# Kernel tuning notes

Hardware: AMD Instinct MI355X
Metric: run time of the kernel (lower is better)

## Reference

```python
import jax, jax.numpy as jnp
import numpy as np

N_NODES = 20000
N_EDGES = 100000
WALK_LEN = 4
FEAT_DIM = 256
HID = 64
NUM_HEAD = 8
H_RNN = NUM_HEAD * HID  # 512
OUT_DIM = 16


def setup_inputs() -> dict:
    key = jax.random.key(0)
    ks = jax.random.split(key, 12)
    s = 0.05  # small init scale for numerical stability
    return {
        "x": jax.random.normal(ks[0], (N_NODES, FEAT_DIM), jnp.float32),
        "W_mlp": jax.random.normal(ks[1], (HID, FEAT_DIM), jnp.float32) * s,
        "b_mlp": jnp.zeros((HID,), jnp.float32),
        "W_ih": jax.random.normal(ks[2], (3 * H_RNN, HID), jnp.float32) * s,
        "W_hh": jax.random.normal(ks[3], (3 * H_RNN, H_RNN), jnp.float32) * s,
        "b_ih": jnp.zeros((3 * H_RNN,), jnp.float32),
        "b_hh": jnp.zeros((3 * H_RNN,), jnp.float32),
        "attn": jax.random.normal(ks[4], (1, NUM_HEAD, HID), jnp.float32) * s,
        "W_emb": jax.random.normal(ks[5], (HID, H_RNN), jnp.float32) * s,
        "b_emb": jnp.zeros((HID,), jnp.float32),
        "W_last": jax.random.normal(ks[6], (OUT_DIM, HID), jnp.float32) * s,
        "b_last": jnp.zeros((OUT_DIM,), jnp.float32),
        "edge_metapath_indices": jax.random.randint(ks[7], (N_EDGES, WALK_LEN), 0, N_NODES),
        "num_nodes": N_NODES,
    }


def reference(x, W_mlp, b_mlp, W_ih, W_hh, b_ih, b_hh, attn, W_emb, b_emb,
              W_last, b_last, edge_metapath_indices, num_nodes):
    # self channel: embedding = mlp(data.x)
    emb = x @ W_mlp.T + b_mlp                       # [N, hid]

    # rnn channel: gather per-metapath node embeddings
    edata = emb[edge_metapath_indices]              # [E, L, hid]
    E = edata.shape[0]
    h_rnn = W_hh.shape[1]

    # torch nn.GRU cell (gate order r, z, n), scan over path length
    def gru_step(h, x_t):
        xg = x_t @ W_ih.T + b_ih                    # [E, 3H]
        hg = h @ W_hh.T + b_hh                      # [E, 3H]
        xr, xz, xn = jnp.split(xg, 3, axis=-1)
        hr, hz, hn = jnp.split(hg, 3, axis=-1)
        r = jax.nn.sigmoid(xr + hr)
        z = jax.nn.sigmoid(xz + hz)
        n = jnp.tanh(xn + r * hn)
        return (1.0 - z) * n + z * h, None

    h0 = jnp.zeros((E, h_rnn), edata.dtype)
    hT, _ = jax.lax.scan(gru_step, h0, jnp.swapaxes(edata, 0, 1))  # [E, 8*hid]

    num_head, hid = attn.shape[1], attn.shape[2]
    eft = hT.reshape(E, num_head, hid)              # per-edge features

    # attention logits + leaky_relu(0.01)
    a = jnp.sum(eft * attn, axis=-1)                # [E, num_head]
    a = jnp.where(a > 0, a, 0.01 * a)

    # edge softmax grouped by destination node (indices[:, -1])
    dst = edge_metapath_indices[:, -1]
    m = jax.ops.segment_max(a, dst, num_segments=num_nodes)        # [N, H]
    ea = jnp.exp(a - m[dst])
    ssum = jax.ops.segment_sum(ea, dst, num_segments=num_nodes)    # [N, H]
    alpha = ea / ssum[dst]                          # [E, H]

    # message passing: scatter-sum of attention-weighted edge features
    ft = jax.ops.segment_sum(eft * alpha[:, :, None], dst,
                             num_segments=num_nodes)               # [N, H, hid]
    ret = ft.reshape(num_nodes, num_head * hid)
    rnn_emb = ret @ W_emb.T + b_emb                 # [N, hid]

    out = rnn_emb @ W_last.T + b_last               # [N, out_dim]
    return out
```

## Files before the change

kernel.cpp:

```cpp
#include <hip/hip_runtime.h>
#include <hip/hip_bf16.h>
#include <cstdint>

#define N_NODES 20000
#define N_EDGES 100000
#define WALK 4
#define FDIM 256
#define HID 64
#define NHEAD 8
#define HR 512
#define OUTD 16

typedef __attribute__((ext_vector_type(8))) short bf16x8;
typedef __attribute__((ext_vector_type(8))) unsigned short u16x8;
typedef __attribute__((ext_vector_type(4))) float f32x4;

__device__ __forceinline__ float b2f(unsigned short u){
  union{float f; unsigned u;} x; x.u = ((unsigned)u)<<16; return x.f;
}
__device__ __forceinline__ unsigned short f2b(float f){
  union{float f; unsigned u;} x; x.f = f;
  unsigned r = x.u + 0x7FFFu + ((x.u>>16)&1u);
  return (unsigned short)(r>>16);
}
__device__ __forceinline__ float sigmoidf_(float v){ return 1.0f/(1.0f+__expf(-v)); }
__device__ __forceinline__ float tanh_c(float v){
  v = fminf(fmaxf(v, -15.f), 15.f);
  const float t2 = __expf(2.0f*v);
  return (t2 - 1.0f) / (t2 + 1.0f);
}

__device__ __forceinline__ void gload16(const void* g, void* l){
  __builtin_amdgcn_global_load_lds(
      (const __attribute__((address_space(1))) void*)(g),
      (__attribute__((address_space(3))) void*)(l),
      16, 0, 0);
}

__device__ __forceinline__ f32x4 mfma16(bf16x8 a, bf16x8 b, f32x4 c){
  return __builtin_amdgcn_mfma_f32_16x16x32_bf16(a, b, c, 0, 0, 0);
}

__launch_bounds__(256)
__global__ void emb_kernel(const float* __restrict__ x,
                           const float* __restrict__ Wm,
                           const float* __restrict__ bm,
                           unsigned short* __restrict__ emb_bf)
{
  __shared__ float xs[4][FDIM];
  const int tid = threadIdx.x;
  const int node0 = blockIdx.x * 4;
  {
    const int row = tid >> 6;
    const int k4  = (tid & 63) * 4;
    *reinterpret_cast<float4*>(&xs[row][k4]) =
      *reinterpret_cast<const float4*>(&x[(size_t)(node0+row)*FDIM + k4]);
  }
  __syncthreads();
  const int nn = tid >> 6, c = tid & 63;
  float acc = bm[c];
  const float* wr = &Wm[c*FDIM];
  #pragma unroll 8
  for (int k=0;k<FDIM;k+=4){
    const float4 w = *reinterpret_cast<const float4*>(&wr[k]);
    acc += xs[nn][k]*w.x + xs[nn][k+1]*w.y + xs[nn][k+2]*w.z + xs[nn][k+3]*w.w;
  }
  emb_bf[(size_t)(node0+nn)*HID + c] = f2b(acc);
}

__launch_bounds__(256)
__global__ void prep_kernel(const float* __restrict__ Whh,
                            const float* __restrict__ Wih,
                            const float* __restrict__ Wemb,
                            unsigned short* __restrict__ WhhP,
                            unsigned short* __restrict__ WihP,
                            unsigned short* __restrict__ WembP)
{
  const int t = blockIdx.x*256 + threadIdx.x;
  if (t < 8*192*512){
    const int k = t & 511;
    const int r = (t >> 9) % 192;
    const int db = t / 98304;
    const int f = r >> 4, fr = r & 15;
    const int g = f % 3, dgrp = f / 3;
    const int G = g*HR + db*64 + dgrp*16 + fr;
    const int kg = k >> 6, kw = k & 63;
    const int c = kw >> 3, o = kw & 7;
    const int ksrc = (kg<<6) + (((c ^ (r&7)) << 3) | o);
    WhhP[t] = f2b(Whh[(size_t)G*HR + ksrc]);
  }
  if (t < 8*192*64){
    const int k = t & 63;
    const int r = (t >> 6) % 192;
    const int db = t / 12288;
    const int f = r >> 4, fr = r & 15;
    const int g = f % 3, dgrp = f / 3;
    const int G = g*HR + db*64 + dgrp*16 + fr;
    const int c = k >> 3, o = k & 7;
    const int ksrc = (((c ^ (r&7)) << 3) | o);
    WihP[t] = f2b(Wih[(size_t)G*HID + ksrc]);
  }
  if (t < 64*512){
    const int k = t & 511;
    const int o = t >> 9;
    const int kg = k >> 6, kw = k & 63;
    const int c = kw >> 3, off = kw & 7;
    const int ksrc = (kg<<6) + (((c ^ (o&7)) << 3) | off);
    WembP[t] = f2b(Wemb[(size_t)o*HR + ksrc]);
  }
}

__launch_bounds__(512)
__global__ void xg_kernel(const unsigned short* __restrict__ emb_bf,
                          const unsigned short* __restrict__ WihP,
                          const float* __restrict__ b_ih,
                          const float* __restrict__ b_hh,
                          unsigned short* __restrict__ xnP,
                          unsigned short* __restrict__ h1n)
{
  __shared__ __align__(16) char smem[32768 + 24576];
  char* Ab = smem;
  char* Bb = smem + 32768;
  const int tid = threadIdx.x, lane = tid & 63, w = tid >> 6;
  const int wr = w >> 1, wn = w & 1;
  const int n0 = blockIdx.x * 256;
  const int db = blockIdx.y;

  #pragma unroll
  for (int j=0;j<4;++j){
    const int flat = j*512 + tid;
    const int row = flat >> 3, c = flat & 7;
    int n = n0 + row; if (n > N_NODES-1) n = N_NODES-1;
    gload16(emb_bf + ((size_t)n*HID + ((c ^ (row&7))<<3)), Ab + ((j*512 + w*64)<<4));
  }
  #pragma unroll
  for (int j=0;j<3;++j){
    const int flat = j*512 + tid;
    const int row = flat >> 3, c = flat & 7;
    gload16(WihP + ((size_t)(db*192 + row)*HID + c*8), Bb + ((j*512 + w*64)<<4));
  }
  asm volatile("s_waitcnt vmcnt(0)" ::: "memory");
  __builtin_amdgcn_s_barrier();

  f32x4 acc[4][6];
  #pragma unroll
  for (int m=0;m<4;++m)
    #pragma unroll
    for (int f=0;f<6;++f) acc[m][f] = (f32x4)(0.f);

  auto readFrag = [&](const char* base, int row, int kk)->bf16x8{
    const int chunk = (kk<<2) + (lane>>4);
    return *reinterpret_cast<const bf16x8*>(base + (row<<7) + ((chunk ^ (row&7))<<4));
  };
  #pragma unroll
  for (int kk=0; kk<2; ++kk){
    bf16x8 a_[4];
    #pragma unroll
    for (int mf=0; mf<4; ++mf) a_[mf] = readFrag(Ab, wr*64 + mf*16 + (lane&15), kk);
    #pragma unroll
    for (int nf=0; nf<6; ++nf){
      const bf16x8 b_ = readFrag(Bb, wn*96 + nf*16 + (lane&15), kk);
      #pragma unroll
      for (int mf=0; mf<4; ++mf) acc[mf][nf] = mfma16(a_[mf], b_, acc[mf][nf]);
    }
  }

  const int fr_ = lane & 15;
  #pragma unroll
  for (int mf=0; mf<4; ++mf){
    #pragma unroll
    for (int reg=0; reg<4; ++reg){
      const int row = wr*64 + mf*16 + ((lane>>4)<<2) + reg;
      const int n = n0 + row;
      if (n < N_NODES){
        #pragma unroll
        for (int t=0; t<2; ++t){
          const int d6 = (2*wn+t)*16 + fr_;
          const int dG = db*64 + d6;
          const float xr = acc[mf][t*3+0][reg] + b_ih[dG];
          const float xz = acc[mf][t*3+1][reg] + b_ih[HR+dG];
          const float xn = acc[mf][t*3+2][reg] + b_ih[2*HR+dG];
          xnP[((size_t)db*N_NODES + n)*64 + d6] = f2b(xn);
          const float r = sigmoidf_(xr + b_hh[dG]);
          const float z = sigmoidf_(xz + b_hh[HR+dG]);
          const float nn = tanh_c(xn + r*b_hh[2*HR+dG]);
          h1n[(size_t)n*HR + dG] = f2b((1.0f - z)*nn);
        }
      }
    }
  }
}

template<int STEP, bool SCORE>
__launch_bounds__(512, 2)
__global__ void gru_mfma(const unsigned short* __restrict__ emb_bf,
                         const int* __restrict__ idx,
                         const unsigned short* __restrict__ h_in,
                         unsigned short* __restrict__ h_out,
                         const unsigned short* __restrict__ WhhP,
                         const unsigned short* __restrict__ WihP,
                         const unsigned short* __restrict__ xnP,
                         const float* __restrict__ b_ih,
                         const float* __restrict__ b_hh,
                         const float* __restrict__ attn,
                         float* __restrict__ a_buf)
{
  constexpr bool GATHER = (STEP == 1);
  __shared__ __align__(16) char smem[3*32768 + 2*24576];

  const int tid = threadIdx.x;
  const int lane = tid & 63;
  const int w = tid >> 6;
  const int wr = w >> 1, wn = w & 1;

  const int bid = blockIdx.x;
  const int sid = (bid & 7)*391 + (bid >> 3);
  const int et = sid >> 3;
  const int db = sid & 7;
  const int e0 = et * 256;

  f32x4 acc[4][6];
  #pragma unroll
  for (int m=0;m<4;++m)
    #pragma unroll
    for (int f=0;f<6;++f) acc[m][f] = (f32x4)(0.f);

  auto Abase = [&](int s)->char*{ return smem + s*32768; };
  auto Bbase = [&](int s)->char*{ return smem + 98304 + s*24576; };

  auto stage_A = [&](int slot, int kt){
    #pragma unroll
    for (int j=0;j<4;++j){
      const int flat = j*512 + tid;
      const int row = flat >> 3, c = flat & 7;
      int e = e0 + row; if (e > N_EDGES-1) e = N_EDGES-1;
      const unsigned short* src;
      if (kt == 8){
        const int node = idx[e*WALK + STEP];
        src = emb_bf + ((size_t)node*HID + ((c ^ (row&7)) << 3));
      } else if (GATHER){
        const int node = idx[e*WALK];
        src = h_in + ((size_t)node*HR + kt*64 + ((c ^ (row&7)) << 3));
      } else {
        src = h_in + ((size_t)e*HR + kt*64 + c*8);
      }
      gload16(src, Abase(slot) + ((j*512 + w*64) << 4));
    }
  };
  auto stage_B = [&](int slot, int kt){
    #pragma unroll
    for (int j=0;j<3;++j){
      const int flat = j*512 + tid;
      const int row = flat >> 3, c = flat & 7;
      const unsigned short* src = (kt < 8)
        ? WhhP + ((size_t)(db*192 + row)*HR + kt*64 + c*8)
        : WihP + ((size_t)(db*192 + row)*HID + c*8);
      gload16(src, Bbase(slot) + ((j*512 + w*64) << 4));
    }
  };

  auto readFrag = [&](const char* base, int row, int kk)->bf16x8{
    const int chunk = (kk<<2) + (lane>>4);
    return *reinterpret_cast<const bf16x8*>(base + (row<<7) + ((chunk ^ (row&7))<<4));
  };

#define COMPUTE(ab, bb, kk, XS)                                               \
  {                                                                           \
    bf16x8 a_[4];                                                             \
    _Pragma("unroll")                                                         \
    for (int mf=0; mf<4; ++mf)                                                \
      a_[mf] = readFrag(ab, wr*64 + mf*16 + (lane&15), kk);                   \
    __builtin_amdgcn_s_setprio(1);                                            \
    _Pragma("unroll")                                                         \
    for (int nf=0; nf<6; ++nf){                                               \
      if (XS && (nf % 3) == 2) continue;                                      \
      const bf16x8 b_ = readFrag(bb, wn*96 + nf*16 + (lane&15), kk);          \
      _Pragma("unroll")                                                       \
      for (int mf=0; mf<4; ++mf)                                              \
        acc[mf][nf] = mfma16(a_[mf], b_, acc[mf][nf]);                        \
    }                                                                         \
    __builtin_amdgcn_s_setprio(0);                                            \
  }

  stage_A(0, 0); stage_B(0, 0); stage_A(1, 1);
  asm volatile("s_waitcnt vmcnt(4)" ::: "memory");
  __builtin_amdgcn_s_barrier();
  __builtin_amdgcn_sched_barrier(0);

  #pragma unroll
  for (int kt=0; kt<9; ++kt){
    char* ab = Abase(kt%3);
    char* bb = Bbase(kt&1);
    if (kt+1 < 9) stage_B((kt+1)&1, kt+1);
    if (kt==8){ COMPUTE(ab, bb, 0, true);  } else { COMPUTE(ab, bb, 0, false); }
    if (kt+2 < 9) stage_A((kt+2)%3, kt+2);
    if (kt==8){ COMPUTE(ab, bb, 1, true);  } else { COMPUTE(ab, bb, 1, false); }
    if (kt < 8){
      if (kt < 7) asm volatile("s_waitcnt vmcnt(4)" ::: "memory");
      else        asm volatile("s_waitcnt vmcnt(0)" ::: "memory");
      __builtin_amdgcn_s_barrier();
      __builtin_amdgcn_sched_barrier(0);
    }
  }
#undef COMPUTE

  const int fr_ = lane & 15;
  float bhr[2], bhz[2], bhn[2], at[2];
  #pragma unroll
  for (int t=0; t<2; ++t){
    const int d6 = (2*wn+t)*16 + fr_;
    const int dG = db*64 + d6;
    bhr[t] = b_ih[dG]      + b_hh[dG];
    bhz[t] = b_ih[HR+dG]   + b_hh[HR+dG];
    bhn[t] = b_hh[2*HR+dG];
    at[t]  = SCORE ? attn[db*HID + d6] : 0.f;
  }

  #pragma unroll
  for (int mf=0; mf<4; ++mf){
    #pragma unroll
    for (int reg=0; reg<4; ++reg){
      const int row = wr*64 + mf*16 + ((lane>>4)<<2) + reg;
      const int e = e0 + row;
      float sp = 0.f;
      if (e < N_EDGES){
        const int4 iv = *reinterpret_cast<const int4*>(&idx[e*WALK]);
        const int nodeS = (STEP==1) ? iv.y : ((STEP==2) ? iv.z : iv.w);
        #pragma unroll
        for (int t=0; t<2; ++t){
          const int d6 = (2*wn+t)*16 + fr_;
          const int dG = db*64 + d6;
          const float xn = b2f(xnP[((size_t)db*N_NODES + nodeS)*64 + d6]);
          float hold;
          if (GATHER) hold = b2f(h_in[(size_t)iv.x*HR + dG]);
          else        hold = b2f(h_in[(size_t)e*HR + db*64 + (((d6>>3) ^ (e&7))<<3) + (d6&7)]);
          const float r  = sigmoidf_(acc[mf][t*3+0][reg] + bhr[t]);
          const float z  = sigmoidf_(acc[mf][t*3+1][reg] + bhz[t]);
          const float hn = acc[mf][t*3+2][reg] + bhn[t];
          const float nn = tanh_c(xn + r*hn);
          const float hv = (1.0f - z)*nn + z*hold;
          h_out[(size_t)e*HR + db*64 + (((d6>>3) ^ (e&7))<<3) + (d6&7)] = f2b(hv);
          if (SCORE) sp += hv * at[t];
        }
      }
      if (SCORE){
        sp += __shfl_xor(sp, 1);
        sp += __shfl_xor(sp, 2);
        sp += __shfl_xor(sp, 4);
        sp += __shfl_xor(sp, 8);
        if (fr_ == 0 && e < N_EDGES)
          atomicAdd(&a_buf[e*NHEAD + db], sp);
      }
    }
  }
}

__launch_bounds__(256)
__global__ void score2_kernel(const int* __restrict__ idx,
                              float* __restrict__ a_buf,
                              unsigned int* __restrict__ mmax)
{
  const int flat = blockIdx.x*256 + threadIdx.x;
  const int e = flat >> 3, h = flat & 7;
  const float s = a_buf[flat];
  const float a = s > 0.f ? s : 0.01f*s;
  a_buf[flat] = a;
  const int dst = idx[e*WALK + 3];
  union{float f; unsigned u;} x; x.f = a;
  const unsigned key = (x.u & 0x80000000u) ? ~x.u : (x.u | 0x80000000u);
  atomicMax(&mmax[dst*NHEAD + h], key);
}

__launch_bounds__(256)
__global__ void ea_kernel(const int* __restrict__ idx,
                          float* __restrict__ a_buf,
                          const unsigned int* __restrict__ mmax,
                          float* __restrict__ ssum)
{
  const int flat = blockIdx.x*256 + threadIdx.x;
  const int e = flat >> 3, h = flat & 7;
  const int dst = idx[e*WALK + 3];
  const unsigned key = mmax[dst*NHEAD + h];
  union{float f; unsigned u;} x;
  x.u = (key & 0x80000000u) ? (key & 0x7FFFFFFFu) : ~key;
  const float ea = __expf(a_buf[flat] - x.f);
  a_buf[flat] = ea;
  atomicAdd(&ssum[dst*NHEAD + h], ea);
}

__launch_bounds__(256)
__global__ void alpha_kernel(const int* __restrict__ idx,
                             float* __restrict__ a_buf,
                             const float* __restrict__ ssum)
{
  const int flat = blockIdx.x*256 + threadIdx.x;
  const int e = flat >> 3, h = flat & 7;
  const int dst = idx[e*WALK + 3];
  a_buf[flat] = a_buf[flat] / ssum[dst*NHEAD + h];
}

__launch_bounds__(256)
__global__ void z_kernel(const unsigned short* __restrict__ hT,
                         const int* __restrict__ idx,
                         const float* __restrict__ alpha,
                         const unsigned short* __restrict__ WembP,
                         float* __restrict__ zacc)
{
  __shared__ __align__(16) char zs[40960];
  char* Az = zs;
  char* Bz = zs + 32768;
  const int tid = threadIdx.x;
  const int lane = tid & 63;
  const int w = tid >> 6;
  const int e0 = blockIdx.x * 256;

  f32x4 acc[4][4];
  #pragma unroll
  for (int m=0;m<4;++m)
    #pragma unroll
    for (int f=0;f<4;++f) acc[m][f] = (f32x4)(0.f);

  auto readFrag = [&](const char* base, int row, int kk)->bf16x8{
    const int chunk = (kk<<2) + (lane>>4);
    return *reinterpret_cast<const bf16x8*>(base + (row<<7) + ((chunk ^ (row&7))<<4));
  };

  #pragma unroll 1
  for (int kt=0; kt<8; ++kt){
    __syncthreads();
    #pragma unroll
    for (int j=0;j<8;++j){
      const int flat = j*256 + tid;
      const int row = flat >> 3, c = flat & 7;
      int e = e0 + row; if (e > N_EDGES-1) e = N_EDGES-1;
      const u16x8 hv = *reinterpret_cast<const u16x8*>(hT + (size_t)e*HR + kt*64 + c*8);
      const float al = alpha[e*NHEAD + kt];
      union { bf16x8 v; unsigned short s[8]; } o;
      #pragma unroll
      for (int i=0;i<8;++i) o.s[i] = f2b(b2f(hv[i]) * al);
      *reinterpret_cast<bf16x8*>(Az + flat*16) = o.v;
    }
    #pragma unroll
    for (int j=0;j<2;++j){
      const int flat = j*256 + tid;
      const int row = flat >> 3, c = flat & 7;
      gload16(WembP + ((size_t)row*HR + kt*64 + c*8), Bz + ((j*256 + w*64)<<4));
    }
    __syncthreads();
    #pragma unroll
    for (int kk=0; kk<2; ++kk){
      bf16x8 a_[4];
      #pragma unroll
      for (int mf=0; mf<4; ++mf)
        a_[mf] = readFrag(Az, w*64 + mf*16 + (lane&15), kk);
      #pragma unroll
      for (int nf=0; nf<4; ++nf){
        const bf16x8 b_ = readFrag(Bz, nf*16 + (lane&15), kk);
        #pragma unroll
        for (int mf=0; mf<4; ++mf)
          acc[mf][nf] = mfma16(a_[mf], b_, acc[mf][nf]);
      }
    }
  }

  #pragma unroll
  for (int mf=0; mf<4; ++mf){
    #pragma unroll
    for (int reg=0; reg<4; ++reg){
      const int row = w*64 + mf*16 + ((lane>>4)<<2) + reg;
      const int e = e0 + row;
      if (e < N_EDGES){
        const int dst = idx[e*WALK + 3];
        #pragma unroll
        for (int nf=0; nf<4; ++nf){
          const int o = nf*16 + (lane&15);
          atomicAdd(&zacc[(size_t)dst*64 + o], acc[mf][nf][reg]);
        }
      }
    }
  }
}

__launch_bounds__(256)
__global__ void out2_kernel(const float* __restrict__ zacc,
                            const float* __restrict__ b_emb,
                            const float* __restrict__ W_last,
                            const float* __restrict__ b_last,
                            float* __restrict__ out)
{
  const int flat = blockIdx.x*256 + threadIdx.x;
  if (flat >= N_NODES*OUTD) return;
  const int n = flat >> 4, o = flat & 15;
  float s = b_last[o];
  const float* zr = &zacc[(size_t)n*64];
  const float* wl = &W_last[o*64];
  #pragma unroll
  for (int k=0;k<64;++k) s += (zr[k] + b_emb[k]) * wl[k];
  out[(size_t)n*OUTD + o] = s;
}

extern "C" void kernel_launch(void* const* d_in, const int* in_sizes, int n_in,
                              void* d_out, int out_size, void* d_ws, size_t ws_size,
                              hipStream_t stream)
{
  (void)in_sizes; (void)n_in; (void)out_size; (void)ws_size;
  const float* x      = (const float*)d_in[0];
  const float* W_mlp  = (const float*)d_in[1];
  const float* b_mlp  = (const float*)d_in[2];
  const float* W_ih   = (const float*)d_in[3];
  const float* W_hh   = (const float*)d_in[4];
  const float* b_ih   = (const float*)d_in[5];
  const float* b_hh   = (const float*)d_in[6];
  const float* attn   = (const float*)d_in[7];
  const float* W_emb  = (const float*)d_in[8];
  const float* b_emb  = (const float*)d_in[9];
  const float* W_last = (const float*)d_in[10];
  const float* b_last = (const float*)d_in[11];
  const int*   idx    = (const int*)d_in[12];
  float* out = (float*)d_out;

  char* ws = (char*)d_ws;
  unsigned short* WhhP   = (unsigned short*)(ws + 0);
  unsigned short* WihP   = (unsigned short*)(ws + 1572864);
  unsigned short* WembP  = (unsigned short*)(ws + 1769472);
  unsigned short* emb_bf = (unsigned short*)(ws + 1835008);
  unsigned short* xnP    = (unsigned short*)(ws + 4395008);
  float*          a_buf  = (float*)(ws + 24875008);
  unsigned int*   mmax   = (unsigned int*)(ws + 28075008);
  float*          ssum   = (float*)(ws + 28715008);
  float*          zacc   = (float*)(ws + 29355008);
  unsigned short* h_a    = (unsigned short*)(ws + 34475008);
  unsigned short* h_b    = (unsigned short*)(ws + 136875008);
  unsigned short* h1n    = h_b;

  hipMemsetAsync(a_buf, 0, 9600000, stream);

  prep_kernel<<<3072, 256, 0, stream>>>(W_hh, W_ih, W_emb, WhhP, WihP, WembP);
  emb_kernel<<<N_NODES/4, 256, 0, stream>>>(x, W_mlp, b_mlp, emb_bf);

  dim3 xgrid(79, 8);
  xg_kernel<<<xgrid, 512, 0, stream>>>(emb_bf, WihP, b_ih, b_hh, xnP, h1n);

  const int NWG = 391*8;
  gru_mfma<1,false><<<NWG, 512, 0, stream>>>(emb_bf, idx, h1n, h_a, WhhP, WihP, xnP, b_ih, b_hh, attn, a_buf);
  gru_mfma<2,false><<<NWG, 512, 0, stream>>>(emb_bf, idx, h_a, h_b, WhhP, WihP, xnP, b_ih, b_hh, attn, a_buf);
  gru_mfma<3,true ><<<NWG, 512, 0, stream>>>(emb_bf, idx, h_b, h_a, WhhP, WihP, xnP, b_ih, b_hh, attn, a_buf);

  score2_kernel<<<N_EDGES*NHEAD/256, 256, 0, stream>>>(idx, a_buf, mmax);
  ea_kernel<<<N_EDGES*NHEAD/256, 256, 0, stream>>>(idx, a_buf, mmax, ssum);
  alpha_kernel<<<N_EDGES*NHEAD/256, 256, 0, stream>>>(idx, a_buf, ssum);
  z_kernel<<<391, 256, 0, stream>>>(h_a, idx, a_buf, WembP, zacc);
  out2_kernel<<<(N_NODES*OUTD+255)/256, 256, 0, stream>>>(zacc, b_emb, W_last, b_last, out);
}
```

Baseline: 1.299 ms.

## Halve GRU edge tile, double-buffer LDS, stage epilogue through LDS for vector stores

The GRU step kernel moves from a 256-edge tile with triple-buffered A to a 128-edge tile with double-buffered A/B, cutting LDS to 80KB and raising launch bounds to 4 blocks per CU. Gather indices are hoisted out of the k-loop into registers. The epilogue now transposes accumulators through LDS so each thread handles one edge and 8 contiguous features, which gives 16-byte vectorized loads and stores and one attention atomic per edge-head instead of a shuffle reduction. In exchange, B-weight reuse per block is halved, so weight traffic doubles, and prefetch depth drops to a single stage with a full vmcnt(0) wait every iteration.

```diff
diff --git a/kernel.cpp b/kernel.cpp
--- a/kernel.cpp
+++ b/kernel.cpp
@@ -192,7 +192,7 @@
 }
 
 template<int STEP, bool SCORE>
-__launch_bounds__(512, 2)
+__launch_bounds__(512, 4)
 __global__ void gru_mfma(const unsigned short* __restrict__ emb_bf,
                          const int* __restrict__ idx,
                          const unsigned short* __restrict__ h_in,
@@ -206,7 +206,7 @@
                          float* __restrict__ a_buf)
 {
   constexpr bool GATHER = (STEP == 1);
-  __shared__ __align__(16) char smem[3*32768 + 2*24576];
+  __shared__ __align__(16) char smem[81920];
 
   const int tid = threadIdx.x;
   const int lane = tid & 63;
@@ -214,35 +214,42 @@
   const int wr = w >> 1, wn = w & 1;
 
   const int bid = blockIdx.x;
-  const int sid = (bid & 7)*391 + (bid >> 3);
+  const int sid = (bid & 7)*782 + (bid >> 3);
   const int et = sid >> 3;
   const int db = sid & 7;
-  const int e0 = et * 256;
-
-  f32x4 acc[4][6];
-  #pragma unroll
-  for (int m=0;m<4;++m)
+  const int e0 = et * 128;
+
+  int eS[2], nH[2], nX[2];
+  #pragma unroll
+  for (int j=0;j<2;++j){
+    int e = e0 + ((j*512 + tid) >> 3);
+    if (e > N_EDGES-1) e = N_EDGES-1;
+    eS[j] = e;
+    nX[j] = idx[e*WALK + STEP];
+    nH[j] = GATHER ? idx[e*WALK] : 0;
+  }
+
+  f32x4 acc[2][6];
+  #pragma unroll
+  for (int m=0;m<2;++m)
     #pragma unroll
     for (int f=0;f<6;++f) acc[m][f] = (f32x4)(0.f);
 
-  auto Abase = [&](int s)->char*{ return smem + s*32768; };
-  auto Bbase = [&](int s)->char*{ return smem + 98304 + s*24576; };
+  auto Abase = [&](int s)->char*{ return smem + s*16384; };
+  auto Bbase = [&](int s)->char*{ return smem + 32768 + s*24576; };
 
   auto stage_A = [&](int slot, int kt){
     #pragma unroll
-    for (int j=0;j<4;++j){
+    for (int j=0;j<2;++j){
       const int flat = j*512 + tid;
       const int row = flat >> 3, c = flat & 7;
-      int e = e0 + row; if (e > N_EDGES-1) e = N_EDGES-1;
       const unsigned short* src;
       if (kt == 8){
-        const int node = idx[e*WALK + STEP];
-        src = emb_bf + ((size_t)node*HID + ((c ^ (row&7)) << 3));
+        src = emb_bf + ((size_t)nX[j]*HID + ((c ^ (row&7)) << 3));
       } else if (GATHER){
-        const int node = idx[e*WALK];
-        src = h_in + ((size_t)node*HR + kt*64 + ((c ^ (row&7)) << 3));
+        src = h_in + ((size_t)nH[j]*HR + kt*64 + ((c ^ (row&7)) << 3));
       } else {
-        src = h_in + ((size_t)e*HR + kt*64 + c*8);
+        src = h_in + ((size_t)eS[j]*HR + kt*64 + c*8);
       }
       gload16(src, Abase(slot) + ((j*512 + w*64) << 4));
     }
@@ -266,92 +273,128 @@
 
 #define COMPUTE(ab, bb, kk, XS)                                               \
   {                                                                           \
-    bf16x8 a_[4];                                                             \
+    bf16x8 a_[2];                                                             \
     _Pragma("unroll")                                                         \
-    for (int mf=0; mf<4; ++mf)                                                \
-      a_[mf] = readFrag(ab, wr*64 + mf*16 + (lane&15), kk);                   \
+    for (int mf=0; mf<2; ++mf)                                                \
+      a_[mf] = readFrag(ab, wr*32 + mf*16 + (lane&15), kk);                   \
     __builtin_amdgcn_s_setprio(1);                                            \
     _Pragma("unroll")                                                         \
     for (int nf=0; nf<6; ++nf){                                               \
       if (XS && (nf % 3) == 2) continue;                                      \
       const bf16x8 b_ = readFrag(bb, wn*96 + nf*16 + (lane&15), kk);          \
       _Pragma("unroll")                                                       \
-      for (int mf=0; mf<4; ++mf)                                              \
+      for (int mf=0; mf<2; ++mf)                                              \
         acc[mf][nf] = mfma16(a_[mf], b_, acc[mf][nf]);                        \
     }                                                                         \
     __builtin_amdgcn_s_setprio(0);                                            \
   }
 
-  stage_A(0, 0); stage_B(0, 0); stage_A(1, 1);
-  asm volatile("s_waitcnt vmcnt(4)" ::: "memory");
+  stage_A(0, 0); stage_B(0, 0);
+  asm volatile("s_waitcnt vmcnt(0)" ::: "memory");
   __builtin_amdgcn_s_barrier();
   __builtin_amdgcn_sched_barrier(0);
 
   #pragma unroll
   for (int kt=0; kt<9; ++kt){
-    char* ab = Abase(kt%3);
-    char* bb = Bbase(kt&1);
-    if (kt+1 < 9) stage_B((kt+1)&1, kt+1);
+    const int buf = kt & 1;
+    char* ab = Abase(buf);
+    char* bb = Bbase(buf);
+    if (kt < 8){ stage_A(buf^1, kt+1); stage_B(buf^1, kt+1); }
     if (kt==8){ COMPUTE(ab, bb, 0, true);  } else { COMPUTE(ab, bb, 0, false); }
-    if (kt+2 < 9) stage_A((kt+2)%3, kt+2);
     if (kt==8){ COMPUTE(ab, bb, 1, true);  } else { COMPUTE(ab, bb, 1, false); }
     if (kt < 8){
-      if (kt < 7) asm volatile("s_waitcnt vmcnt(4)" ::: "memory");
-      else        asm volatile("s_waitcnt vmcnt(0)" ::: "memory");
+      asm volatile("s_waitcnt vmcnt(0)" ::: "memory");
       __builtin_amdgcn_s_barrier();
       __builtin_amdgcn_sched_barrier(0);
     }
   }
 #undef COMPUTE
 
-  const int fr_ = lane & 15;
-  float bhr[2], bhz[2], bhn[2], at[2];
-  #pragma unroll
-  for (int t=0; t<2; ++t){
-    const int d6 = (2*wn+t)*16 + fr_;
-    const int dG = db*64 + d6;
-    bhr[t] = b_ih[dG]      + b_hh[dG];
-    bhz[t] = b_ih[HR+dG]   + b_hh[HR+dG];
-    bhn[t] = b_hh[2*HR+dG];
-    at[t]  = SCORE ? attn[db*HID + d6] : 0.f;
-  }
-
-  #pragma unroll
-  for (int mf=0; mf<4; ++mf){
-    #pragma unroll
-    for (int reg=0; reg<4; ++reg){
-      const int row = wr*64 + mf*16 + ((lane>>4)<<2) + reg;
-      const int e = e0 + row;
-      float sp = 0.f;
-      if (e < N_EDGES){
-        const int4 iv = *reinterpret_cast<const int4*>(&idx[e*WALK]);
-        const int nodeS = (STEP==1) ? iv.y : ((STEP==2) ? iv.z : iv.w);
+  float* EX = (float*)smem;
+  const int eL = tid & 127;
+  const int c4 = tid >> 7;
+  const int tt = c4 >> 1;
+  const int fr0 = (c4 & 1) * 8;
+  const int eg = e0 + eL;
+  const int ec = (eg > N_EDGES-1) ? (N_EDGES-1) : eg;
+  float spart = 0.f;
+
+  __syncthreads();
+
+  #pragma unroll
+  for (int p=0; p<2; ++p){
+    if (p) __syncthreads();
+    if (wn == p){
+      #pragma unroll
+      for (int mf=0; mf<2; ++mf){
+        const int rc = wr*8 + mf*4 + (lane>>4);
         #pragma unroll
-        for (int t=0; t<2; ++t){
-          const int d6 = (2*wn+t)*16 + fr_;
-          const int dG = db*64 + d6;
-          const float xn = b2f(xnP[((size_t)db*N_NODES + nodeS)*64 + d6]);
-          float hold;
-          if (GATHER) hold = b2f(h_in[(size_t)iv.x*HR + dG]);
-          else        hold = b2f(h_in[(size_t)e*HR + db*64 + (((d6>>3) ^ (e&7))<<3) + (d6&7)]);
-          const float r  = sigmoidf_(acc[mf][t*3+0][reg] + bhr[t]);
-          const float z  = sigmoidf_(acc[mf][t*3+1][reg] + bhz[t]);
-          const float hn = acc[mf][t*3+2][reg] + bhn[t];
-          const float nn = tanh_c(xn + r*hn);
-          const float hv = (1.0f - z)*nn + z*hold;
-          h_out[(size_t)e*HR + db*64 + (((d6>>3) ^ (e&7))<<3) + (d6&7)] = f2b(hv);
-          if (SCORE) sp += hv * at[t];
+        for (int nf=0; nf<6; ++nf){
+          const int cl = nf*16 + (lane&15);
+          *reinterpret_cast<f32x4*>((char*)EX + cl*512 + ((rc ^ (cl&7))<<4)) = acc[mf][nf];
         }
       }
-      if (SCORE){
-        sp += __shfl_xor(sp, 1);
-        sp += __shfl_xor(sp, 2);
-        sp += __shfl_xor(sp, 4);
-        sp += __shfl_xor(sp, 8);
-        if (fr_ == 0 && e < N_EDGES)
-          atomicAdd(&a_buf[e*NHEAD + db], sp);
-      }
-    }
+    }
+    __syncthreads();
+
+    const int d60 = p*32 + c4*8;
+    const int dG0 = db*64 + d60;
+
+    float gr[8], gz[8], gn[8];
+    #pragma unroll
+    for (int i=0;i<8;++i){
+      const int clr = (tt*3+0)*16 + fr0 + i;
+      const int clz = (tt*3+1)*16 + fr0 + i;
+      const int cln = (tt*3+2)*16 + fr0 + i;
+      const int psw = ((eL>>2) ^ i) << 4;
+      const int wo  = (eL&3) * 4;
+      gr[i] = *reinterpret_cast<const float*>((char*)EX + clr*512 + psw + wo);
+      gz[i] = *reinterpret_cast<const float*>((char*)EX + clz*512 + psw + wo);
+      gn[i] = *reinterpret_cast<const float*>((char*)EX + cln*512 + psw + wo);
+    }
+
+    float bir[8], biz[8], bhn[8];
+    #pragma unroll
+    for (int i=0;i<8;++i){
+      bir[i] = b_ih[dG0+i]      + b_hh[dG0+i];
+      biz[i] = b_ih[HR+dG0+i]   + b_hh[HR+dG0+i];
+      bhn[i] = b_hh[2*HR+dG0+i];
+    }
+
+    const int nodeS = idx[ec*WALK + STEP];
+    const u16x8 xnv = *reinterpret_cast<const u16x8*>(
+        xnP + ((size_t)db*N_NODES + nodeS)*64 + d60);
+    u16x8 hov;
+    if (GATHER){
+      const int nodeH = idx[ec*WALK];
+      hov = *reinterpret_cast<const u16x8*>(h_in + (size_t)nodeH*HR + dG0);
+    } else {
+      const int cidx = d60 >> 3;
+      hov = *reinterpret_cast<const u16x8*>(
+          h_in + (size_t)ec*HR + db*64 + ((cidx ^ (ec&7))<<3));
+    }
+
+    union { u16x8 v; unsigned short s[8]; } outp;
+    #pragma unroll
+    for (int i=0;i<8;++i){
+      const float r  = sigmoidf_(gr[i] + bir[i]);
+      const float z  = sigmoidf_(gz[i] + biz[i]);
+      const float hn = gn[i] + bhn[i];
+      const float xn = b2f(xnv[i]);
+      const float nn = tanh_c(xn + r*hn);
+      const float hv = (1.0f - z)*nn + z*b2f(hov[i]);
+      outp.s[i] = f2b(hv);
+      if (SCORE) spart += hv * attn[dG0 + i];
+    }
+    if (eg < N_EDGES){
+      const int cidx = d60 >> 3;
+      *reinterpret_cast<u16x8*>(
+          h_out + (size_t)eg*HR + db*64 + ((cidx ^ (eg&7))<<3)) = outp.v;
+    }
+  }
+
+  if (SCORE && eg < N_EDGES){
+    atomicAdd(&a_buf[eg*NHEAD + db], spart);
   }
 }
 
@@ -541,7 +584,7 @@
   dim3 xgrid(79, 8);
   xg_kernel<<<xgrid, 512, 0, stream>>>(emb_bf, WihP, b_ih, b_hh, xnP, h1n);
 
-  const int NWG = 391*8;
+  const int NWG = 782*8;
   gru_mfma<1,false><<<NWG, 512, 0, stream>>>(emb_bf, idx, h1n, h_a, WhhP, WihP, xnP, b_ih, b_hh, attn, a_buf);
   gru_mfma<2,false><<<NWG, 512, 0, stream>>>(emb_bf, idx, h_a, h_b, WhhP, WihP, xnP, b_ih, b_hh, attn, a_buf);
   gru_mfma<3,true ><<<NWG, 512, 0, stream>>>(emb_bf, idx, h_b, h_a, WhhP, WihP, xnP, b_ih, b_hh, attn, a_buf);
```

Measured after the change: 1.340 ms. +3.2%, slower.

## Fuse three GRU step kernels into one with the hidden state kept in LDS

Applied to the files above, without the earlier changes.

Replaces the three per-step GRU MFMA launches with a single kernel. Each block owns 64 edges, keeps their 512-wide hidden state in shared memory across all three steps, and writes only the final state to global memory. The input-gate projections for all three gates are now precomputed per node in xg_kernel and gathered in the epilogue, instead of folding W_ih into the GEMM K-loop. This removes the global write/read round trips of the hidden state between steps. In exchange, every block streams the full W_hh once per step, which greatly increases weight traffic. The smaller per-wave MFMA tiles, the barrier on every K-slice and the large LDS footprint (limiting occupancy) may also cut throughput.

```diff
diff --git a/kernel.cpp b/kernel.cpp
--- a/kernel.cpp
+++ b/kernel.cpp
@@ -115,7 +115,7 @@
                           const unsigned short* __restrict__ WihP,
                           const float* __restrict__ b_ih,
                           const float* __restrict__ b_hh,
-                          unsigned short* __restrict__ xnP,
+                          unsigned short* __restrict__ xgP,
                           unsigned short* __restrict__ h1n)
 {
   __shared__ __align__(16) char smem[32768 + 24576];
@@ -180,7 +180,9 @@
           const float xr = acc[mf][t*3+0][reg] + b_ih[dG];
           const float xz = acc[mf][t*3+1][reg] + b_ih[HR+dG];
           const float xn = acc[mf][t*3+2][reg] + b_ih[2*HR+dG];
-          xnP[((size_t)db*N_NODES + n)*64 + d6] = f2b(xn);
+          xgP[(size_t)n*1536 + dG]        = f2b(xr);
+          xgP[(size_t)n*1536 + 512 + dG]  = f2b(xz);
+          xgP[(size_t)n*1536 + 1024 + dG] = f2b(xn);
           const float r = sigmoidf_(xr + b_hh[dG]);
           const float z = sigmoidf_(xz + b_hh[HR+dG]);
           const float nn = tanh_c(xn + r*b_hh[2*HR+dG]);
@@ -191,166 +193,169 @@
   }
 }
 
-template<int STEP, bool SCORE>
 __launch_bounds__(512, 2)
-__global__ void gru_mfma(const unsigned short* __restrict__ emb_bf,
-                         const int* __restrict__ idx,
-                         const unsigned short* __restrict__ h_in,
-                         unsigned short* __restrict__ h_out,
-                         const unsigned short* __restrict__ WhhP,
-                         const unsigned short* __restrict__ WihP,
-                         const unsigned short* __restrict__ xnP,
-                         const float* __restrict__ b_ih,
-                         const float* __restrict__ b_hh,
-                         const float* __restrict__ attn,
-                         float* __restrict__ a_buf)
-{
-  constexpr bool GATHER = (STEP == 1);
-  __shared__ __align__(16) char smem[3*32768 + 2*24576];
-
-  const int tid = threadIdx.x;
-  const int lane = tid & 63;
-  const int w = tid >> 6;
-  const int wr = w >> 1, wn = w & 1;
-
-  const int bid = blockIdx.x;
-  const int sid = (bid & 7)*391 + (bid >> 3);
-  const int et = sid >> 3;
-  const int db = sid & 7;
-  const int e0 = et * 256;
-
-  f32x4 acc[4][6];
-  #pragma unroll
-  for (int m=0;m<4;++m)
-    #pragma unroll
-    for (int f=0;f<6;++f) acc[m][f] = (f32x4)(0.f);
-
-  auto Abase = [&](int s)->char*{ return smem + s*32768; };
-  auto Bbase = [&](int s)->char*{ return smem + 98304 + s*24576; };
-
-  auto stage_A = [&](int slot, int kt){
-    #pragma unroll
-    for (int j=0;j<4;++j){
-      const int flat = j*512 + tid;
-      const int row = flat >> 3, c = flat & 7;
-      int e = e0 + row; if (e > N_EDGES-1) e = N_EDGES-1;
-      const unsigned short* src;
-      if (kt == 8){
-        const int node = idx[e*WALK + STEP];
-        src = emb_bf + ((size_t)node*HID + ((c ^ (row&7)) << 3));
-      } else if (GATHER){
-        const int node = idx[e*WALK];
-        src = h_in + ((size_t)node*HR + kt*64 + ((c ^ (row&7)) << 3));
-      } else {
-        src = h_in + ((size_t)e*HR + kt*64 + c*8);
-      }
-      gload16(src, Abase(slot) + ((j*512 + w*64) << 4));
-    }
+__global__ void gru_fused(const int* __restrict__ idx,
+                          const unsigned short* __restrict__ h1n,
+                          const unsigned short* __restrict__ WhhP,
+                          const unsigned short* __restrict__ xgP,
+                          const float* __restrict__ b_hh,
+                          const float* __restrict__ attn,
+                          unsigned short* __restrict__ hT,
+                          float* __restrict__ a_buf)
+{
+  __shared__ __align__(16) char smem[147456];
+  char* const hL = smem;
+  float* const biasT = (float*)(smem + 139264);
+  float* const attnT = (float*)(smem + 145408);
+
+  const int tid = threadIdx.x, lane = tid & 63, w = tid >> 6;
+  const int lrow = lane & 15, lkg = lane >> 4;
+  const int rg = w >> 2, dgrp = w & 3;
+  const int e0 = blockIdx.x * 64;
+
+  auto Bbuf = [&](int s)->char*{ return smem + 65536 + s*24576; };
+
+  biasT[tid]      = b_hh[tid];
+  biasT[512+tid]  = b_hh[HR+tid];
+  biasT[1024+tid] = b_hh[2*HR+tid];
+  attnT[tid]      = attn[tid];
+
+  #pragma unroll
+  for (int j=0;j<8;++j){
+    const int flat = j*512 + tid;
+    const int row = flat >> 6, c64 = flat & 63;
+    int e = e0 + row; if (e > N_EDGES-1) e = N_EDGES-1;
+    const int n0 = idx[e*WALK];
+    const u16x8 v = *reinterpret_cast<const u16x8*>(h1n + (size_t)n0*HR + c64*8);
+    *reinterpret_cast<u16x8*>(hL + row*1024 + (c64>>3)*128 + (((c64&7) ^ (row&7))<<4)) = v;
+  }
+  __syncthreads();
+
+  auto readA = [&](int row, int kt, int kk)->bf16x8{
+    return *reinterpret_cast<const bf16x8*>(
+        hL + row*1024 + kt*128 + (((lkg + kk*4) ^ (row&7))<<4));
   };
-  auto stage_B = [&](int slot, int kt){
+  auto readB = [&](const char* bb, int r, int kk)->bf16x8{
+    return *reinterpret_cast<const bf16x8*>(
+        bb + r*128 + (((lkg + kk*4) ^ (r&7))<<4));
+  };
+  auto stageB = [&](int slot, int db, int kt){
     #pragma unroll
     for (int j=0;j<3;++j){
       const int flat = j*512 + tid;
-      const int row = flat >> 3, c = flat & 7;
-      const unsigned short* src = (kt < 8)
-        ? WhhP + ((size_t)(db*192 + row)*HR + kt*64 + c*8)
-        : WihP + ((size_t)(db*192 + row)*HID + c*8);
-      gload16(src, Bbase(slot) + ((j*512 + w*64) << 4));
+      const int r = flat >> 3, c = flat & 7;
+      gload16(WhhP + ((size_t)(db*192 + r)*HR + kt*64 + c*8),
+              Bbuf(slot) + ((j*512 + w*64) << 4));
     }
   };
 
-  auto readFrag = [&](const char* base, int row, int kk)->bf16x8{
-    const int chunk = (kk<<2) + (lane>>4);
-    return *reinterpret_cast<const bf16x8*>(base + (row<<7) + ((chunk ^ (row&7))<<4));
-  };
-
-#define COMPUTE(ab, bb, kk, XS)                                               \
-  {                                                                           \
-    bf16x8 a_[4];                                                             \
-    _Pragma("unroll")                                                         \
-    for (int mf=0; mf<4; ++mf)                                                \
-      a_[mf] = readFrag(ab, wr*64 + mf*16 + (lane&15), kk);                   \
-    __builtin_amdgcn_s_setprio(1);                                            \
-    _Pragma("unroll")                                                         \
-    for (int nf=0; nf<6; ++nf){                                               \
-      if (XS && (nf % 3) == 2) continue;                                      \
-      const bf16x8 b_ = readFrag(bb, wn*96 + nf*16 + (lane&15), kk);          \
-      _Pragma("unroll")                                                       \
-      for (int mf=0; mf<4; ++mf)                                              \
-        acc[mf][nf] = mfma16(a_[mf], b_, acc[mf][nf]);                        \
-    }                                                                         \
-    __builtin_amdgcn_s_setprio(0);                                            \
-  }
-
-  stage_A(0, 0); stage_B(0, 0); stage_A(1, 1);
-  asm volatile("s_waitcnt vmcnt(4)" ::: "memory");
-  __builtin_amdgcn_s_barrier();
-  __builtin_amdgcn_sched_barrier(0);
-
-  #pragma unroll
-  for (int kt=0; kt<9; ++kt){
-    char* ab = Abase(kt%3);
-    char* bb = Bbase(kt&1);
-    if (kt+1 < 9) stage_B((kt+1)&1, kt+1);
-    if (kt==8){ COMPUTE(ab, bb, 0, true);  } else { COMPUTE(ab, bb, 0, false); }
-    if (kt+2 < 9) stage_A((kt+2)%3, kt+2);
-    if (kt==8){ COMPUTE(ab, bb, 1, true);  } else { COMPUTE(ab, bb, 1, false); }
-    if (kt < 8){
-      if (kt < 7) asm volatile("s_waitcnt vmcnt(4)" ::: "memory");
-      else        asm volatile("s_waitcnt vmcnt(0)" ::: "memory");
-      __builtin_amdgcn_s_barrier();
-      __builtin_amdgcn_sched_barrier(0);
-    }
-  }
-#undef COMPUTE
-
-  const int fr_ = lane & 15;
-  float bhr[2], bhz[2], bhn[2], at[2];
-  #pragma unroll
-  for (int t=0; t<2; ++t){
-    const int d6 = (2*wn+t)*16 + fr_;
-    const int dG = db*64 + d6;
-    bhr[t] = b_ih[dG]      + b_hh[dG];
-    bhz[t] = b_ih[HR+dG]   + b_hh[HR+dG];
-    bhn[t] = b_hh[2*HR+dG];
-    at[t]  = SCORE ? attn[db*HID + d6] : 0.f;
-  }
-
-  #pragma unroll
-  for (int mf=0; mf<4; ++mf){
-    #pragma unroll
-    for (int reg=0; reg<4; ++reg){
-      const int row = wr*64 + mf*16 + ((lane>>4)<<2) + reg;
-      const int e = e0 + row;
-      float sp = 0.f;
-      if (e < N_EDGES){
-        const int4 iv = *reinterpret_cast<const int4*>(&idx[e*WALK]);
-        const int nodeS = (STEP==1) ? iv.y : ((STEP==2) ? iv.z : iv.w);
-        #pragma unroll
-        for (int t=0; t<2; ++t){
-          const int d6 = (2*wn+t)*16 + fr_;
-          const int dG = db*64 + d6;
-          const float xn = b2f(xnP[((size_t)db*N_NODES + nodeS)*64 + d6]);
-          float hold;
-          if (GATHER) hold = b2f(h_in[(size_t)iv.x*HR + dG]);
-          else        hold = b2f(h_in[(size_t)e*HR + db*64 + (((d6>>3) ^ (e&7))<<3) + (d6&7)]);
-          const float r  = sigmoidf_(acc[mf][t*3+0][reg] + bhr[t]);
-          const float z  = sigmoidf_(acc[mf][t*3+1][reg] + bhz[t]);
-          const float hn = acc[mf][t*3+2][reg] + bhn[t];
-          const float nn = tanh_c(xn + r*hn);
-          const float hv = (1.0f - z)*nn + z*hold;
-          h_out[(size_t)e*HR + db*64 + (((d6>>3) ^ (e&7))<<3) + (d6&7)] = f2b(hv);
-          if (SCORE) sp += hv * at[t];
+  float hsv[8][8];
+
+  #pragma unroll 1
+  for (int t=1; t<WALK; ++t){
+    int nodes[2][4];
+    #pragma unroll
+    for (int mf=0;mf<2;++mf)
+      #pragma unroll
+      for (int reg=0;reg<4;++reg){
+        int e = e0 + rg*32 + mf*16 + lkg*4 + reg;
+        if (e > N_EDGES-1) e = N_EDGES-1;
+        nodes[mf][reg] = idx[e*WALK + t];
+      }
+
+    #pragma unroll
+    for (int db=0; db<8; ++db){
+      f32x4 acc[2][3];
+      #pragma unroll
+      for (int m=0;m<2;++m)
+        #pragma unroll
+        for (int g=0;g<3;++g) acc[m][g] = (f32x4)(0.f);
+
+      stageB(0, db, 0); stageB(1, db, 1);
+
+      #pragma unroll 1
+      for (int kt=0; kt<8; ++kt){
+        if (kt == 7) asm volatile("s_waitcnt vmcnt(0)" ::: "memory");
+        else         asm volatile("s_waitcnt vmcnt(3)" ::: "memory");
+        __builtin_amdgcn_s_barrier();
+        __builtin_amdgcn_sched_barrier(0);
+        if (kt + 2 < 8) stageB((kt+2)%3, db, kt+2);
+        char* bb = Bbuf(kt%3);
+        #pragma unroll
+        for (int kk=0; kk<2; ++kk){
+          const bf16x8 a0 = readA(rg*32 + lrow,      kt, kk);
+          const bf16x8 a1 = readA(rg*32 + 16 + lrow, kt, kk);
+          __builtin_amdgcn_s_setprio(1);
+          #pragma unroll
+          for (int g=0; g<3; ++g){
+            const bf16x8 b_ = readB(bb, (dgrp*3+g)*16 + lrow, kk);
+            acc[0][g] = mfma16(a0, b_, acc[0][g]);
+            acc[1][g] = mfma16(a1, b_, acc[1][g]);
+          }
+          __builtin_amdgcn_s_setprio(0);
         }
       }
-      if (SCORE){
-        sp += __shfl_xor(sp, 1);
-        sp += __shfl_xor(sp, 2);
-        sp += __shfl_xor(sp, 4);
-        sp += __shfl_xor(sp, 8);
-        if (fr_ == 0 && e < N_EDGES)
-          atomicAdd(&a_buf[e*NHEAD + db], sp);
+      __builtin_amdgcn_s_barrier();
+
+      const int col = db*64 + dgrp*16 + lrow;
+      const float br = biasT[col], bz = biasT[512+col], bn = biasT[1024+col];
+      const float av = attnT[col];
+      #pragma unroll
+      for (int mf=0;mf<2;++mf){
+        #pragma unroll
+        for (int reg=0;reg<4;++reg){
+          const int row = rg*32 + mf*16 + lkg*4 + reg;
+          const int node = nodes[mf][reg];
+          const size_t xb = (size_t)node*1536 + col;
+          const float xr = b2f(xgP[xb]);
+          const float xz = b2f(xgP[xb + 512]);
+          const float xn = b2f(xgP[xb + 1024]);
+          const float hold = b2f(*reinterpret_cast<const unsigned short*>(
+              hL + row*1024 + db*128 + ((((col>>3)&7) ^ (row&7))<<4) + (col&7)*2));
+          const float r  = sigmoidf_(xr + acc[mf][0][reg] + br);
+          const float z  = sigmoidf_(xz + acc[mf][1][reg] + bz);
+          const float nn = tanh_c(xn + r*(acc[mf][2][reg] + bn));
+          const float hv = (1.0f - z)*nn + z*hold;
+          hsv[db][mf*4+reg] = hv;
+          if (t == WALK-1){
+            float s = hv * av;
+            s += __shfl_xor(s, 1);
+            s += __shfl_xor(s, 2);
+            s += __shfl_xor(s, 4);
+            s += __shfl_xor(s, 8);
+            const int e = e0 + row;
+            if (lrow == mf*4+reg && e < N_EDGES)
+              atomicAdd(&a_buf[e*NHEAD + db], s);
+          }
+        }
       }
+    }
+
+    __syncthreads();
+    #pragma unroll
+    for (int db=0; db<8; ++db){
+      const int col = db*64 + dgrp*16 + lrow;
+      #pragma unroll
+      for (int mf=0;mf<2;++mf)
+        #pragma unroll
+        for (int reg=0;reg<4;++reg){
+          const int row = rg*32 + mf*16 + lkg*4 + reg;
+          *reinterpret_cast<unsigned short*>(
+              hL + row*1024 + db*128 + ((((col>>3)&7) ^ (row&7))<<4) + (col&7)*2)
+            = f2b(hsv[db][mf*4+reg]);
+        }
+    }
+    __syncthreads();
+  }
+
+  #pragma unroll
+  for (int j=0;j<8;++j){
+    const int flat = j*512 + tid;
+    const int row = flat >> 6;
+    const int e = e0 + row;
+    if (e < N_EDGES){
+      const u16x8 v = *reinterpret_cast<const u16x8*>(hL + flat*16);
+      *reinterpret_cast<u16x8*>(hT + (size_t)e*HR + (flat&63)*8) = v;
     }
   }
 }
@@ -524,14 +529,13 @@
   unsigned short* WihP   = (unsigned short*)(ws + 1572864);
   unsigned short* WembP  = (unsigned short*)(ws + 1769472);
   unsigned short* emb_bf = (unsigned short*)(ws + 1835008);
-  unsigned short* xnP    = (unsigned short*)(ws + 4395008);
-  float*          a_buf  = (float*)(ws + 24875008);
-  unsigned int*   mmax   = (unsigned int*)(ws + 28075008);
-  float*          ssum   = (float*)(ws + 28715008);
-  float*          zacc   = (float*)(ws + 29355008);
-  unsigned short* h_a    = (unsigned short*)(ws + 34475008);
-  unsigned short* h_b    = (unsigned short*)(ws + 136875008);
-  unsigned short* h1n    = h_b;
+  unsigned short* h1n    = (unsigned short*)(ws + 4395008);
+  unsigned short* xgP    = (unsigned short*)(ws + 24875008);
+  float*          a_buf  = (float*)(ws + 86315008);
+  unsigned int*   mmax   = (unsigned int*)(ws + 89515008);
+  float*          ssum   = (float*)(ws + 90155008);
+  float*          zacc   = (float*)(ws + 90795008);
+  unsigned short* hT     = (unsigned short*)(ws + 95915008);
 
   hipMemsetAsync(a_buf, 0, 9600000, stream);
 
@@ -539,16 +543,14 @@
   emb_kernel<<<N_NODES/4, 256, 0, stream>>>(x, W_mlp, b_mlp, emb_bf);
 
   dim3 xgrid(79, 8);
-  xg_kernel<<<xgrid, 512, 0, stream>>>(emb_bf, WihP, b_ih, b_hh, xnP, h1n);
-
-  const int NWG = 391*8;
-  gru_mfma<1,false><<<NWG, 512, 0, stream>>>(emb_bf, idx, h1n, h_a, WhhP, WihP, xnP, b_ih, b_hh, attn, a_buf);
-  gru_mfma<2,false><<<NWG, 512, 0, stream>>>(emb_bf, idx, h_a, h_b, WhhP, WihP, xnP, b_ih, b_hh, attn, a_buf);
-  gru_mfma<3,true ><<<NWG, 512, 0, stream>>>(emb_bf, idx, h_b, h_a, WhhP, WihP, xnP, b_ih, b_hh, attn, a_buf);
+  xg_kernel<<<xgrid, 512, 0, stream>>>(emb_bf, WihP, b_ih, b_hh, xgP, h1n);
+
+  const int NB = (N_EDGES + 63) / 64;
+  gru_fused<<<NB, 512, 0, stream>>>(idx, h1n, WhhP, xgP, b_hh, attn, hT, a_buf);
 
   score2_kernel<<<N_EDGES*NHEAD/256, 256, 0, stream>>>(idx, a_buf, mmax);
   ea_kernel<<<N_EDGES*NHEAD/256, 256, 0, stream>>>(idx, a_buf, mmax, ssum);
   alpha_kernel<<<N_EDGES*NHEAD/256, 256, 0, stream>>>(idx, a_buf, ssum);
-  z_kernel<<<391, 256, 0, stream>>>(h_a, idx, a_buf, WembP, zacc);
+  z_kernel<<<391, 256, 0, stream>>>(hT, idx, a_buf, WembP, zacc);
   out2_kernel<<<(N_NODES*OUTD+255)/256, 256, 0, stream>>>(zacc, b_emb, W_last, b_last, out);
 }
```

Result: slower. 2.163 ms (+66.5%).
